# Performance work log

Hardware: AMD Instinct MI355X
Metric: run time of the kernel (lower is better)

## Reference

```python
import jax, jax.numpy as jnp
import numpy as np
from jax import lax

N = 100000      # nodes
E = 1600000     # edges
F_IN = 128      # nfeat
F_OUT = 32      # nhid


def _l2norm(v, eps=1e-12):
    return v / jnp.maximum(jnp.linalg.norm(v), eps)


def setup_inputs() -> dict:
    key = jax.random.key(0)
    k1, k2, k3, k4, k5 = jax.random.split(key, 5)
    x = jax.random.normal(k1, (N, F_IN), dtype=jnp.float32)
    edge_index = jax.random.randint(k2, (2, E), 0, N, dtype=jnp.int64)
    W = jax.random.normal(k3, (F_OUT, F_IN), dtype=jnp.float32) * (1.0 / np.sqrt(F_IN))
    bias = jax.random.normal(k4, (F_OUT,), dtype=jnp.float32) * 0.01
    prelu_a = jnp.full((1,), 0.25, dtype=jnp.float32)  # PReLU default init
    u_sn = jax.random.normal(k5, (F_OUT,), dtype=jnp.float32)
    return {"x": x, "edge_index": edge_index, "W": W, "bias": bias,
            "prelu_a": prelu_a, "u_sn": u_sn}


def _spectral_norm_weight(W, u):
    # one power iteration (torch default), u/v treated as buffers (no grad)
    v = lax.stop_gradient(_l2norm(W.T @ u))
    u2 = lax.stop_gradient(_l2norm(W @ v))
    sigma = jnp.dot(u2, W @ v)
    return W / sigma


def reference(x, edge_index, W, bias, prelu_a, u_sn):
    W_sn = _spectral_norm_weight(W, u_sn)
    # linear transform first (PyG GCNConv): [N, F_OUT]
    xw = x @ W_sn.T
    # add self loops
    loop = jnp.arange(N, dtype=edge_index.dtype)
    row = jnp.concatenate([edge_index[0], loop])  # source
    col = jnp.concatenate([edge_index[1], loop])  # target
    # symmetric normalization deg^{-1/2} A deg^{-1/2}, deg over targets
    deg = jax.ops.segment_sum(jnp.ones_like(col, dtype=xw.dtype), col, num_segments=N)
    dis = jnp.where(deg > 0, lax.rsqrt(deg), 0.0)
    norm = dis[row] * dis[col]                    # [E+N]
    # gather-scale-scatter aggregation
    msgs = xw[row] * norm[:, None]                # [E+N, F_OUT]
    out = jax.ops.segment_sum(msgs, col, num_segments=N)
    out = out + bias
    # PReLU with single shared slope
    a = prelu_a[0]
    return jnp.where(out >= 0, out, a * out)
```

## Files before the change

kernel.cpp:

```cpp
#include <hip/hip_runtime.h>
#include <hip/hip_fp16.h>

#define F_IN 128
#define F_OUT 32
#define PBLK 512
#define BSH 8
#define BMSK 255
#define MAXB 512

__global__ __launch_bounds__(256) void k_hist(const int* __restrict__ col,
                                              int* __restrict__ M, int E_, int NB) {
    __shared__ int h[MAXB];
    int p = blockIdx.x, t = threadIdx.x;
    for (int b = t; b < NB; b += 256) h[b] = 0;
    __syncthreads();
    int epb = (E_ + PBLK - 1) / PBLK;
    int e0 = p * epb, e1 = min(e0 + epb, E_);
    for (int e = e0 + t; e < e1; e += 256)
        atomicAdd(&h[col[e] >> BSH], 1);
    __syncthreads();
    for (int b = t; b < NB; b += 256) M[(size_t)b * PBLK + p] = h[b];
}

__global__ __launch_bounds__(256) void k_scanA(int* __restrict__ M,
                                               int* __restrict__ total, int NB) {
    __shared__ int sd[256];
    int b = blockIdx.x, t = threadIdx.x;
    int v0 = M[(size_t)b * PBLK + 2 * t];
    int v1 = M[(size_t)b * PBLK + 2 * t + 1];
    int s = v0 + v1;
    sd[t] = s;
    __syncthreads();
    for (int o = 1; o < 256; o <<= 1) {
        int u = (t >= o) ? sd[t - o] : 0;
        __syncthreads();
        sd[t] += u;
        __syncthreads();
    }
    int cb = sd[t] - s;
    M[(size_t)b * PBLK + 2 * t]     = cb;
    M[(size_t)b * PBLK + 2 * t + 1] = cb + v0;
    if (t == 255) total[b] = sd[255];
}

__global__ __launch_bounds__(256) void k_scat1(
    const int* __restrict__ ei, const int* __restrict__ M,
    const int* __restrict__ total, int* __restrict__ base,
    unsigned* __restrict__ staging, int E_, int NB) {
    __shared__ int scur[MAXB];
    __shared__ int sd[256];
    int p = blockIdx.x, t = threadIdx.x;
    int C = (NB + 255) >> 8;
    int vals[2];
    int run = 0;
    for (int j = 0; j < C; ++j) {
        int b = t * C + j;
        int v = (b < NB) ? total[b] : 0;
        vals[j] = run;
        run += v;
    }
    int tsum = run;
    sd[t] = tsum;
    __syncthreads();
    for (int o = 1; o < 256; o <<= 1) {
        int u = (t >= o) ? sd[t - o] : 0;
        __syncthreads();
        sd[t] += u;
        __syncthreads();
    }
    int cb = sd[t] - tsum;
    for (int j = 0; j < C; ++j) {
        int b = t * C + j;
        if (b < NB) {
            int sb = cb + vals[j];
            scur[b] = sb + M[(size_t)b * PBLK + p];
            if (p == 0) base[b] = sb;
        }
    }
    if (p == 0 && t == 255) base[NB] = sd[255];
    __syncthreads();
    int epb = (E_ + PBLK - 1) / PBLK;
    int e0 = p * epb, e1 = min(e0 + epb, E_);
    const int* col = ei + E_;
    for (int e = e0 + t; e < e1; e += 256) {
        int c = col[e];
        int r = ei[e];
        int pos = atomicAdd(&scur[c >> BSH], 1);
        staging[pos] = ((unsigned)r << BSH) | (unsigned)(c & BMSK);
    }
}

__global__ __launch_bounds__(512) void k_sort2(
    const unsigned* __restrict__ staging, const int* __restrict__ base,
    int* __restrict__ esr, float* __restrict__ dis,
    int* __restrict__ cursor, int Nn, int E_, int NB) {
    __shared__ int hist[256];
    __shared__ int sd[256];
    __shared__ int lcur[256];
    int b = blockIdx.x, t = threadIdx.x;
    int nb0 = b << BSH;
    int nc = min(1 << BSH, Nn - nb0);
    if (t < 256) hist[t] = 0;
    __syncthreads();
    int s0 = base[b], s1 = base[b + 1];
    for (int j = s0 + t; j < s1; j += 512)
        atomicAdd(&hist[staging[j] & BMSK], 1);
    __syncthreads();
    int h = 0;
    if (t < 256) {
        h = hist[t];
        if (t < nc) dis[nb0 + t] = rsqrtf((float)h + 1.0f);
        sd[t] = h;
    }
    __syncthreads();
    for (int o = 1; o < 256; o <<= 1) {
        int u = 0;
        if (t < 256 && t >= o) u = sd[t - o];
        __syncthreads();
        if (t < 256) sd[t] += u;
        __syncthreads();
    }
    if (t < 256) {
        int excl = sd[t] - h;
        if (t < nc) cursor[nb0 + t] = s0 + excl;
        lcur[t] = s0 + excl;
    }
    if (b == NB - 1 && t == 0) cursor[Nn] = E_;
    __syncthreads();
    for (int j = s0 + t; j < s1; j += 512) {
        unsigned v = staging[j];
        int pp = atomicAdd(&lcur[v & BMSK], 1);
        esr[pp] = (int)(v >> BSH);
    }
}

__global__ __launch_bounds__(256) void k1_xw(
    const float* __restrict__ x, const float* __restrict__ W,
    const float* __restrict__ u, const float* __restrict__ dis,
    __half* __restrict__ xwh, int Nn) {
    __shared__ float xs[128 * 65];
    __shared__ float wt[128 * 32];
    __shared__ float sv[F_IN];
    __shared__ float sr[F_IN];
    __shared__ float ssc;
    int t = threadIdx.x;

    if (t < F_IN) {
        float a = 0.f;
        for (int i = 0; i < F_OUT; ++i) a += W[i * F_IN + t] * u[i];
        sv[t] = a; sr[t] = a * a;
    }
    __syncthreads();
    for (int o = 64; o > 0; o >>= 1) {
        if (t < o) sr[t] += sr[t + o];
        __syncthreads();
    }
    if (t == 0) ssc = 1.0f / fmaxf(sqrtf(sr[0]), 1e-12f);
    __syncthreads();
    if (t < F_IN) sv[t] *= ssc;
    __syncthreads();
    if (t < F_OUT) {
        float a = 0.f;
        for (int j = 0; j < F_IN; ++j) a += W[t * F_IN + j] * sv[j];
        sr[t] = a * a;
    }
    __syncthreads();
    for (int o = 16; o > 0; o >>= 1) {
        if (t < o) sr[t] += sr[t + o];
        __syncthreads();
    }
    if (t == 0) ssc = 1.0f / fmaxf(sqrtf(sr[0]), 1e-30f);
    __syncthreads();
    float is = ssc;

    int rbase = blockIdx.x * 128;
    {
        int f = t >> 3;
        int kb = 16 * (t & 7);
        const float4* wrow = (const float4*)(W + (size_t)f * F_IN + kb);
#pragma unroll
        for (int j = 0; j < 4; ++j) {
            float4 w = wrow[j];
            int k = kb + 4 * j;
            wt[(k + 0) * 32 + f] = w.x * is;
            wt[(k + 1) * 32 + f] = w.y * is;
            wt[(k + 2) * 32 + f] = w.z * is;
            wt[(k + 3) * 32 + f] = w.w * is;
        }
    }

    int r0 = (t >> 3) * 4;
    int f0 = (t & 7) * 4;
    float4 acc0 = {0, 0, 0, 0}, acc1 = {0, 0, 0, 0};
    float4 acc2 = {0, 0, 0, 0}, acc3 = {0, 0, 0, 0};
    const float4* wt4 = (const float4*)wt;
    int fq = f0 >> 2;

    for (int kc = 0; kc < 2; ++kc) {
        __syncthreads();
        {
            int rr = t >> 4;
            int k0 = 4 * (t & 15);
#pragma unroll
            for (int pi = 0; pi < 8; ++pi) {
                int r = pi * 16 + rr;
                int grow = rbase + r;
                if (grow >= Nn) grow = Nn - 1;
                float4 v = *(const float4*)(x + (size_t)grow * F_IN + kc * 64 + k0);
                xs[r * 65 + k0 + 0] = v.x;
                xs[r * 65 + k0 + 1] = v.y;
                xs[r * 65 + k0 + 2] = v.z;
                xs[r * 65 + k0 + 3] = v.w;
            }
        }
        __syncthreads();
#pragma unroll 4
        for (int kk = 0; kk < 64; ++kk) {
            int k = kc * 64 + kk;
            float4 w = wt4[k * 8 + fq];
            float x0 = xs[(r0 + 0) * 65 + kk];
            float x1 = xs[(r0 + 1) * 65 + kk];
            float x2 = xs[(r0 + 2) * 65 + kk];
            float x3 = xs[(r0 + 3) * 65 + kk];
            acc0.x += x0 * w.x; acc0.y += x0 * w.y; acc0.z += x0 * w.z; acc0.w += x0 * w.w;
            acc1.x += x1 * w.x; acc1.y += x1 * w.y; acc1.z += x1 * w.z; acc1.w += x1 * w.w;
            acc2.x += x2 * w.x; acc2.y += x2 * w.y; acc2.z += x2 * w.z; acc2.w += x2 * w.w;
            acc3.x += x3 * w.x; acc3.y += x3 * w.y; acc3.z += x3 * w.z; acc3.w += x3 * w.w;
        }
    }
    int g0 = rbase + r0;
#pragma unroll
    for (int q = 0; q < 4; ++q) {
        int g = g0 + q;
        if (g < Nn) {
            float d = dis[g];
            float4 a = (q == 0) ? acc0 : (q == 1) ? acc1 : (q == 2) ? acc2 : acc3;
            ushort4 s;
            s.x = __half_as_ushort(__float2half(a.x * d));
            s.y = __half_as_ushort(__float2half(a.y * d));
            s.z = __half_as_ushort(__float2half(a.z * d));
            s.w = __half_as_ushort(__float2half(a.w * d));
            *(ushort4*)(xwh + (size_t)g * F_OUT + f0) = s;
        }
    }
}

__device__ __forceinline__ void acc_row(const __half* xws, int r, int f4, float4& acc) {
    uint2 raw = *((const uint2*)(xws + (size_t)r * F_OUT) + f4);
    __half2 h0 = *reinterpret_cast<__half2*>(&raw.x);
    __half2 h1 = *reinterpret_cast<__half2*>(&raw.y);
    float2 fa = __half22float2(h0);
    float2 fb = __half22float2(h1);
    acc.x += fa.x; acc.y += fa.y; acc.z += fb.x; acc.w += fb.y;
}

__global__ __launch_bounds__(512) void k_gather(
    const int* __restrict__ esr, const int* __restrict__ cursor,
    const __half* __restrict__ xws, const float* __restrict__ dis,
    const float* __restrict__ bias, const float* __restrict__ pa,
    float* __restrict__ out, int Nn) {
    int t = threadIdx.x;
    int node = blockIdx.x * 64 + (t >> 3);
    if (node >= Nn) return;
    int f4 = t & 7;
    int start = cursor[node], end = cursor[node + 1];
    float4 acc = {0, 0, 0, 0};
    int j0 = start;
    for (; j0 + 8 <= end; j0 += 8) {
        int rf = esr[j0 + f4];
        int r0 = __shfl(rf, 0, 8), r1 = __shfl(rf, 1, 8);
        int r2 = __shfl(rf, 2, 8), r3 = __shfl(rf, 3, 8);
        int r4 = __shfl(rf, 4, 8), r5 = __shfl(rf, 5, 8);
        int r6 = __shfl(rf, 6, 8), r7 = __shfl(rf, 7, 8);
        acc_row(xws, r0, f4, acc); acc_row(xws, r1, f4, acc);
        acc_row(xws, r2, f4, acc); acc_row(xws, r3, f4, acc);
        acc_row(xws, r4, f4, acc); acc_row(xws, r5, f4, acc);
        acc_row(xws, r6, f4, acc); acc_row(xws, r7, f4, acc);
    }
    if (j0 < end) {
        int idx = j0 + f4;
        int rf = (idx < end) ? esr[idx] : 0;
        int m = end - j0;
        for (int i = 0; i < m; ++i) {
            int r = __shfl(rf, i, 8);
            acc_row(xws, r, f4, acc);
        }
    }
    float dc = dis[node];
    float4 self;
    {
        uint2 raw = *((const uint2*)(xws + (size_t)node * F_OUT) + f4);
        __half2 h0 = *reinterpret_cast<__half2*>(&raw.x);
        __half2 h1 = *reinterpret_cast<__half2*>(&raw.y);
        float2 fa = __half22float2(h0);
        float2 fb = __half22float2(h1);
        self = make_float4(fa.x, fa.y, fb.x, fb.y);
    }
    float4 bi = *((const float4*)bias + f4);
    float a = pa[0];
    float4 o;
    o.x = (acc.x + self.x) * dc + bi.x;
    o.y = (acc.y + self.y) * dc + bi.y;
    o.z = (acc.z + self.z) * dc + bi.z;
    o.w = (acc.w + self.w) * dc + bi.w;
    o.x = (o.x >= 0.f) ? o.x : a * o.x;
    o.y = (o.y >= 0.f) ? o.y : a * o.y;
    o.z = (o.z >= 0.f) ? o.z : a * o.z;
    o.w = (o.w >= 0.f) ? o.w : a * o.w;
    *((float4*)(out + (size_t)node * F_OUT) + f4) = o;
}

__global__ void k0_specnorm(const float* __restrict__ W, const float* __restrict__ u,
                            float* __restrict__ Wsc) {
    __shared__ float v[F_IN];
    __shared__ float red[F_IN];
    __shared__ float scal;
    int t = threadIdx.x;
    float acc = 0.f;
    for (int i = 0; i < F_OUT; ++i) acc += W[i * F_IN + t] * u[i];
    v[t] = acc; red[t] = acc * acc;
    __syncthreads();
    if (t == 0) {
        float s = 0.f;
        for (int i = 0; i < F_IN; ++i) s += red[i];
        scal = 1.0f / fmaxf(sqrtf(s), 1e-12f);
    }
    __syncthreads();
    v[t] *= scal;
    __syncthreads();
    if (t < F_OUT) {
        float a2 = 0.f;
        for (int j = 0; j < F_IN; ++j) a2 += W[t * F_IN + j] * v[j];
        red[t] = a2 * a2;
    }
    __syncthreads();
    if (t == 0) {
        float s = 0.f;
        for (int i = 0; i < F_OUT; ++i) s += red[i];
        scal = 1.0f / fmaxf(sqrtf(s), 1e-30f);
    }
    __syncthreads();
    float is = scal;
    for (int i = 0; i < F_OUT; ++i)
        Wsc[i * F_IN + t] = W[i * F_IN + t] * is;
}

__global__ void k1_xw_f32(const float* __restrict__ x, const float* __restrict__ Wsc,
                          const float* __restrict__ dis, float* __restrict__ xw, int Nn) {
    int id = blockIdx.x * blockDim.x + threadIdx.x;
    if (id >= Nn * F_OUT) return;
    int r = id >> 5, f = id & 31;
    const float4* x4 = (const float4*)(x + (size_t)r * F_IN);
    const float4* w4 = (const float4*)(Wsc + (size_t)f * F_IN);
    float acc = 0.f;
#pragma unroll
    for (int k = 0; k < F_IN / 4; ++k) {
        float4 a = x4[k];
        float4 b = w4[k];
        acc += a.x * b.x + a.y * b.y + a.z * b.z + a.w * b.w;
    }
    xw[id] = acc * dis[r];
}

__global__ void k2_deg(const int* __restrict__ col, int* __restrict__ cnt, int E_) {
    int e = blockIdx.x * blockDim.x + threadIdx.x;
    if (e < E_) atomicAdd(&cnt[col[e]], 1);
}

__global__ void k3_dis(const int* __restrict__ cnt, float* __restrict__ dis, int Nn) {
    int i = blockIdx.x * blockDim.x + threadIdx.x;
    if (i < Nn) dis[i] = rsqrtf((float)cnt[i] + 1.0f);
}

__global__ void k4_scatter(const int* __restrict__ ei, const float* __restrict__ xws,
                           const float* __restrict__ dis, float* __restrict__ out, int E_) {
    int id = blockIdx.x * blockDim.x + threadIdx.x;
    if (id >= E_ * F_OUT) return;
    int e = id >> 5, f = id & 31;
    int r = ei[e];
    int c = ei[E_ + e];
    atomicAdd(&out[(size_t)c * F_OUT + f], xws[(size_t)r * F_OUT + f] * dis[c]);
}

__global__ void k5_epi(const float* __restrict__ xws, const float* __restrict__ dis,
                       const float* __restrict__ bias, const float* __restrict__ pa,
                       float* __restrict__ out, int Nn) {
    int id = blockIdx.x * blockDim.x + threadIdx.x;
    if (id >= Nn * F_OUT) return;
    int i = id >> 5, f = id & 31;
    float d = dis[i];
    float v = out[id] + xws[id] * d + bias[f];
    float a = pa[0];
    out[id] = (v >= 0.f) ? v : a * v;
}

extern "C" void kernel_launch(void* const* d_in, const int* in_sizes, int n_in,
                              void* d_out, int out_size, void* d_ws, size_t ws_size,
                              hipStream_t stream) {
    const float* x    = (const float*)d_in[0];
    const int*   ei   = (const int*)d_in[1];
    const float* W    = (const float*)d_in[2];
    const float* bias = (const float*)d_in[3];
    const float* pa   = (const float*)d_in[4];
    const float* u    = (const float*)d_in[5];

    int Nn = in_sizes[0] / F_IN;
    int E_ = in_sizes[1] / 2;
    float* out = (float*)d_out;

    int NB = (Nn + BMSK) >> BSH;

    size_t o = 0;
    __half*   xwh     = (__half*)d_ws;       o += (size_t)Nn * (F_OUT / 2);
    float*    dis     = (float*)d_ws + o;    o += Nn;
    int*      cursor  = (int*)d_ws + o;      o += Nn + 1;
    int*      M       = (int*)d_ws + o;      o += (size_t)NB * PBLK;
    int*      total   = (int*)d_ws + o;      o += NB;
    int*      base    = (int*)d_ws + o;      o += NB + 1;
    unsigned* staging = (unsigned*)d_ws + o; o += E_;
    int*      esr     = (int*)d_ws + o;      o += E_;
    bool big_ws = (ws_size >= o * sizeof(float)) && (NB <= MAXB);

    if (big_ws) {
        k_hist<<<PBLK, 256, 0, stream>>>(ei + E_, M, E_, NB);
        k_scanA<<<NB, 256, 0, stream>>>(M, total, NB);
        k_scat1<<<PBLK, 256, 0, stream>>>(ei, M, total, base, staging, E_, NB);
        k_sort2<<<NB, 512, 0, stream>>>(staging, base, esr, dis, cursor, Nn, E_, NB);
        k1_xw<<<(Nn + 127) / 128, 256, 0, stream>>>(x, W, u, dis, xwh, Nn);
        k_gather<<<(Nn + 63) / 64, 512, 0, stream>>>(esr, cursor, xwh, dis, bias, pa, out, Nn);
    } else {
        size_t o2 = 0;
        float* xw2  = (float*)d_ws;       o2 += (size_t)Nn * F_OUT;
        float* Wsc2 = (float*)d_ws + o2;  o2 += F_OUT * F_IN;
        float* dis2 = (float*)d_ws + o2;  o2 += Nn;
        int*   deg2 = (int*)d_ws + o2;    o2 += Nn;
        hipMemsetAsync(deg2, 0, (size_t)Nn * sizeof(int), stream);
        hipMemsetAsync(d_out, 0, (size_t)Nn * F_OUT * sizeof(float), stream);
        k0_specnorm<<<1, 128, 0, stream>>>(W, u, Wsc2);
        k2_deg<<<(E_ + 255) / 256, 256, 0, stream>>>(ei + E_, deg2, E_);
        k3_dis<<<(Nn + 255) / 256, 256, 0, stream>>>(deg2, dis2, Nn);
        int nT1 = Nn * F_OUT;
        k1_xw_f32<<<(nT1 + 255) / 256, 256, 0, stream>>>(x, Wsc2, dis2, xw2, Nn);
        int nT4 = E_ * F_OUT;
        k4_scatter<<<(nT4 + 255) / 256, 256, 0, stream>>>(ei, xw2, dis2, out, E_);
        k5_epi<<<(nT1 + 255) / 256, 256, 0, stream>>>(xw2, dis2, bias, pa, out, Nn);
    }
}
```

Measured before the change: 176.5 us.

## Fuse bucket sort into gather via shared-memory edge indices

Splits the old sort kernel into a degree/cursor pass and moves the per-bucket counting sort into the gather kernel. Each block sorts its bucket's staged edges into a shared-memory index array and aggregates directly from it, which avoids writing and re-reading the global esr array. A global-memory fallback handles buckets larger than the shared capacity. The costs are that only 391 blocks of 512 threads now run the gather, where there were about 1563 before, and that the roughly 48KB of shared memory per block lowers occupancy.

```diff
diff --git a/kernel.cpp b/kernel.cpp
--- a/kernel.cpp
+++ b/kernel.cpp
@@ -7,6 +7,7 @@
 #define BSH 8
 #define BMSK 255
 #define MAXB 512
+#define SCAP 12288
 
 __global__ __launch_bounds__(256) void k_hist(const int* __restrict__ col,
                                               int* __restrict__ M, int E_, int NB) {
@@ -90,13 +91,11 @@
     }
 }
 
-__global__ __launch_bounds__(512) void k_sort2(
+__global__ __launch_bounds__(512) void k_deg(
     const unsigned* __restrict__ staging, const int* __restrict__ base,
-    int* __restrict__ esr, float* __restrict__ dis,
-    int* __restrict__ cursor, int Nn, int E_, int NB) {
+    float* __restrict__ dis, int* __restrict__ cursor, int Nn, int E_, int NB) {
     __shared__ int hist[256];
     __shared__ int sd[256];
-    __shared__ int lcur[256];
     int b = blockIdx.x, t = threadIdx.x;
     int nb0 = b << BSH;
     int nc = min(1 << BSH, Nn - nb0);
@@ -120,18 +119,8 @@
         if (t < 256) sd[t] += u;
         __syncthreads();
     }
-    if (t < 256) {
-        int excl = sd[t] - h;
-        if (t < nc) cursor[nb0 + t] = s0 + excl;
-        lcur[t] = s0 + excl;
-    }
+    if (t < 256 && t < nc) cursor[nb0 + t] = s0 + sd[t] - h;
     if (b == NB - 1 && t == 0) cursor[Nn] = E_;
-    __syncthreads();
-    for (int j = s0 + t; j < s1; j += 512) {
-        unsigned v = staging[j];
-        int pp = atomicAdd(&lcur[v & BMSK], 1);
-        esr[pp] = (int)(v >> BSH);
-    }
 }
 
 __global__ __launch_bounds__(256) void k1_xw(
@@ -254,60 +243,109 @@
     acc.x += fa.x; acc.y += fa.y; acc.z += fb.x; acc.w += fb.y;
 }
 
-__global__ __launch_bounds__(512) void k_gather(
-    const int* __restrict__ esr, const int* __restrict__ cursor,
-    const __half* __restrict__ xws, const float* __restrict__ dis,
+__global__ __launch_bounds__(512) void k_sortgather(
+    const unsigned* __restrict__ staging, const int* __restrict__ base,
+    const int* __restrict__ cursor, const __half* __restrict__ xws,
     const float* __restrict__ bias, const float* __restrict__ pa,
-    float* __restrict__ out, int Nn) {
-    int t = threadIdx.x;
-    int node = blockIdx.x * 64 + (t >> 3);
-    if (node >= Nn) return;
-    int f4 = t & 7;
-    int start = cursor[node], end = cursor[node + 1];
-    float4 acc = {0, 0, 0, 0};
-    int j0 = start;
-    for (; j0 + 8 <= end; j0 += 8) {
-        int rf = esr[j0 + f4];
-        int r0 = __shfl(rf, 0, 8), r1 = __shfl(rf, 1, 8);
-        int r2 = __shfl(rf, 2, 8), r3 = __shfl(rf, 3, 8);
-        int r4 = __shfl(rf, 4, 8), r5 = __shfl(rf, 5, 8);
-        int r6 = __shfl(rf, 6, 8), r7 = __shfl(rf, 7, 8);
-        acc_row(xws, r0, f4, acc); acc_row(xws, r1, f4, acc);
-        acc_row(xws, r2, f4, acc); acc_row(xws, r3, f4, acc);
-        acc_row(xws, r4, f4, acc); acc_row(xws, r5, f4, acc);
-        acc_row(xws, r6, f4, acc); acc_row(xws, r7, f4, acc);
-    }
-    if (j0 < end) {
-        int idx = j0 + f4;
-        int rf = (idx < end) ? esr[idx] : 0;
-        int m = end - j0;
-        for (int i = 0; i < m; ++i) {
-            int r = __shfl(rf, i, 8);
-            acc_row(xws, r, f4, acc);
-        }
-    }
-    float dc = dis[node];
-    float4 self;
-    {
-        uint2 raw = *((const uint2*)(xws + (size_t)node * F_OUT) + f4);
-        __half2 h0 = *reinterpret_cast<__half2*>(&raw.x);
-        __half2 h1 = *reinterpret_cast<__half2*>(&raw.y);
-        float2 fa = __half22float2(h0);
-        float2 fb = __half22float2(h1);
-        self = make_float4(fa.x, fa.y, fb.x, fb.y);
-    }
-    float4 bi = *((const float4*)bias + f4);
-    float a = pa[0];
-    float4 o;
-    o.x = (acc.x + self.x) * dc + bi.x;
-    o.y = (acc.y + self.y) * dc + bi.y;
-    o.z = (acc.z + self.z) * dc + bi.z;
-    o.w = (acc.w + self.w) * dc + bi.w;
-    o.x = (o.x >= 0.f) ? o.x : a * o.x;
-    o.y = (o.y >= 0.f) ? o.y : a * o.y;
-    o.z = (o.z >= 0.f) ? o.z : a * o.z;
-    o.w = (o.w >= 0.f) ? o.w : a * o.w;
-    *((float4*)(out + (size_t)node * F_OUT) + f4) = o;
+    float* __restrict__ out, int* __restrict__ esr, int Nn, int E_, int NB) {
+    __shared__ int sidx[SCAP];
+    __shared__ int cst[257];
+    __shared__ int lcur[256];
+    int b = blockIdx.x, t = threadIdx.x;
+    int nb0 = b << BSH;
+    int nc = min(1 << BSH, Nn - nb0);
+    int s0 = base[b], s1 = base[b + 1];
+    int seg = s1 - s0;
+    if (t < 256) {
+        int v = (t < nc) ? (cursor[nb0 + t] - s0) : seg;
+        cst[t] = v;
+        lcur[t] = v;
+    }
+    if (t == 0) cst[256] = seg;
+    __syncthreads();
+
+    if (seg <= SCAP) {
+        for (int j = s0 + t; j < s1; j += 512) {
+            unsigned v = staging[j];
+            int p = atomicAdd(&lcur[v & BMSK], 1);
+            sidx[p] = (int)(v >> BSH);
+        }
+        __syncthreads();
+        int g = t >> 3, l = t & 7;
+        float aslope = pa[0];
+        float4 bi = *((const float4*)bias + l);
+        for (int n = g; n < nc; n += 64) {
+            int c0 = cst[n], c1 = cst[n + 1];
+            float4 acc = {0, 0, 0, 0};
+            int j = c0;
+            for (; j + 8 <= c1; j += 8) {
+                int r0 = sidx[j + 0], r1 = sidx[j + 1];
+                int r2 = sidx[j + 2], r3 = sidx[j + 3];
+                int r4 = sidx[j + 4], r5 = sidx[j + 5];
+                int r6 = sidx[j + 6], r7 = sidx[j + 7];
+                acc_row(xws, r0, l, acc); acc_row(xws, r1, l, acc);
+                acc_row(xws, r2, l, acc); acc_row(xws, r3, l, acc);
+                acc_row(xws, r4, l, acc); acc_row(xws, r5, l, acc);
+                acc_row(xws, r6, l, acc); acc_row(xws, r7, l, acc);
+            }
+            for (; j < c1; ++j) acc_row(xws, sidx[j], l, acc);
+            float dc = rsqrtf((float)(c1 - c0) + 1.0f);
+            float4 self;
+            {
+                uint2 raw = *((const uint2*)(xws + (size_t)(nb0 + n) * F_OUT) + l);
+                __half2 h0 = *reinterpret_cast<__half2*>(&raw.x);
+                __half2 h1 = *reinterpret_cast<__half2*>(&raw.y);
+                float2 fa = __half22float2(h0);
+                float2 fb = __half22float2(h1);
+                self = make_float4(fa.x, fa.y, fb.x, fb.y);
+            }
+            float4 o;
+            o.x = (acc.x + self.x) * dc + bi.x;
+            o.y = (acc.y + self.y) * dc + bi.y;
+            o.z = (acc.z + self.z) * dc + bi.z;
+            o.w = (acc.w + self.w) * dc + bi.w;
+            o.x = (o.x >= 0.f) ? o.x : aslope * o.x;
+            o.y = (o.y >= 0.f) ? o.y : aslope * o.y;
+            o.z = (o.z >= 0.f) ? o.z : aslope * o.z;
+            o.w = (o.w >= 0.f) ? o.w : aslope * o.w;
+            *((float4*)(out + (size_t)(nb0 + n) * F_OUT) + l) = o;
+        }
+    } else {
+        for (int j = s0 + t; j < s1; j += 512) {
+            unsigned v = staging[j];
+            int p = atomicAdd(&lcur[v & BMSK], 1);
+            esr[s0 + p] = (int)(v >> BSH);
+        }
+        __syncthreads();
+        int g = t >> 3, l = t & 7;
+        float aslope = pa[0];
+        float4 bi = *((const float4*)bias + l);
+        for (int n = g; n < nc; n += 64) {
+            int c0 = cst[n], c1 = cst[n + 1];
+            float4 acc = {0, 0, 0, 0};
+            for (int j = c0; j < c1; ++j) acc_row(xws, esr[s0 + j], l, acc);
+            float dc = rsqrtf((float)(c1 - c0) + 1.0f);
+            float4 self;
+            {
+                uint2 raw = *((const uint2*)(xws + (size_t)(nb0 + n) * F_OUT) + l);
+                __half2 h0 = *reinterpret_cast<__half2*>(&raw.x);
+                __half2 h1 = *reinterpret_cast<__half2*>(&raw.y);
+                float2 fa = __half22float2(h0);
+                float2 fb = __half22float2(h1);
+                self = make_float4(fa.x, fa.y, fb.x, fb.y);
+            }
+            float4 o;
+            o.x = (acc.x + self.x) * dc + bi.x;
+            o.y = (acc.y + self.y) * dc + bi.y;
+            o.z = (acc.z + self.z) * dc + bi.z;
+            o.w = (acc.w + self.w) * dc + bi.w;
+            o.x = (o.x >= 0.f) ? o.x : aslope * o.x;
+            o.y = (o.y >= 0.f) ? o.y : aslope * o.y;
+            o.z = (o.z >= 0.f) ? o.z : aslope * o.z;
+            o.w = (o.w >= 0.f) ? o.w : aslope * o.w;
+            *((float4*)(out + (size_t)(nb0 + n) * F_OUT) + l) = o;
+        }
+    }
 }
 
 __global__ void k0_specnorm(const float* __restrict__ W, const float* __restrict__ u,
@@ -425,9 +463,10 @@
         k_hist<<<PBLK, 256, 0, stream>>>(ei + E_, M, E_, NB);
         k_scanA<<<NB, 256, 0, stream>>>(M, total, NB);
         k_scat1<<<PBLK, 256, 0, stream>>>(ei, M, total, base, staging, E_, NB);
-        k_sort2<<<NB, 512, 0, stream>>>(staging, base, esr, dis, cursor, Nn, E_, NB);
+        k_deg<<<NB, 512, 0, stream>>>(staging, base, dis, cursor, Nn, E_, NB);
         k1_xw<<<(Nn + 127) / 128, 256, 0, stream>>>(x, W, u, dis, xwh, Nn);
-        k_gather<<<(Nn + 63) / 64, 512, 0, stream>>>(esr, cursor, xwh, dis, bias, pa, out, Nn);
+        k_sortgather<<<NB, 512, 0, stream>>>(staging, base, cursor, xwh, bias, pa,
+                                             out, esr, Nn, E_, NB);
     } else {
         size_t o2 = 0;
         float* xw2  = (float*)d_ws;       o2 += (size_t)Nn * F_OUT;
```

Measured after the change: 175.2 us. No clear change (-0.7%).
